# Optimization experiments

Hardware: AMD Instinct MI355X
Metric: run time of the kernel (lower is better)

The kernel has to match this reference:

```python
import jax, jax.numpy as jnp
import numpy as np
import itertools


def _rotation_perms():
    """The 24 rotation matrices of the cube, as permutations of the group
    acting on itself by left multiplication (regular action)."""
    mats = []
    for perm in itertools.permutations(range(3)):
        for signs in itertoolsools if False else itertools.product((1, -1), repeat=3):
            M = np.zeros((3, 3), dtype=np.int64)
            for r, (p, s) in enumerate(zip(perm, signs)):
                M[r, p] = s
            if int(round(np.linalg.det(M))) == 1:
                mats.append(M)
    assert len(mats) == 24
    idx = {m.tobytes(): k for k, m in enumerate(mats)}
    perms = np.zeros((24, 24), dtype=np.int64)
    for k, g in enumerate(mats):
        for i, h in enumerate(mats):
            perms[k, i] = idx[(g @ h).tobytes()]
    return perms


def compute_pair_orbits():
    all_rot = _rotation_perms()
    pair_orbit = np.full((24, 24), -1, dtype=np.int64)
    orbit_id = 0
    for i in range(24):
        for j in range(24):
            if pair_orbit[i, j] == -1:
                for g in all_rot:
                    gi, gj = int(g[i]), int(g[j])
                    if pair_orbit[gi, gj] == -1:
                        pair_orbit[gi, gj] = orbit_id
                orbit_id += 1
    assert (pair_orbit >= 0).all()
    return pair_orbit, orbit_id


C_IN, C_OUT, BATCH = 512, 512, 2048


def setup_inputs() -> dict:
    key = jax.random.key(0)
    kx, kw = jax.random.split(key)
    pair_orbit, n_orbits = compute_pair_orbits()  # (24,24), n_orbits == 24
    x = jax.random.normal(kx, (BATCH, 24, C_IN), dtype=jnp.float32)
    # kaiming-uniform-like init, bound = sqrt(6 / ((1+5) * fan_in)), fan_in = c_in*n_orbits
    bound = float(np.sqrt(1.0 / (C_IN * n_orbits)))
    weight = jax.random.uniform(kw, (C_OUT, C_IN, n_orbits), dtype=jnp.float32,
                                minval=-bound, maxval=bound)
    bias = jnp.zeros((C_OUT,), dtype=jnp.float32)
    return {"x": x, "weight": weight, "bias": bias,
            "pair_orbit": jnp.asarray(pair_orbit)}


def reference(x, weight, bias, pair_orbit):
    # kernel[o, c, i, j] = weight[o, c, pair_orbit[i, j]]
    kernel = weight[:, :, pair_orbit]            # (c_out, c_in, 24, 24)
    out = jnp.einsum('bjc,ocij->bio', x, kernel)  # (batch, 24, c_out)
    return out + bias
```

## Files before the change

kernel.cpp:

```cpp
#include <hip/hip_runtime.h>

#define BATCH 2048
#define CIN   512
#define COUT  512
#define GSZ   24
#define NORB  24
#define M_DIM (BATCH*GSZ)
#define K_DIM (GSZ*CIN)
#define N_DIM COUT
#define BM 192
#define BN 128
#define BK 64

typedef __bf16 bf16x8 __attribute__((ext_vector_type(8)));
typedef float  f32x4  __attribute__((ext_vector_type(4)));
typedef unsigned short u16;

__device__ __forceinline__ u16 f2bf(float f) {
  union { float f; unsigned u; } v; v.f = f;
  unsigned u = v.u;
  return (u16)((u + 0x7fffu + ((u >> 16) & 1u)) >> 16);
}

__global__ void convert_x(const float* __restrict__ x, u16* __restrict__ xb, int n4) {
  int t = blockIdx.x * blockDim.x + threadIdx.x;
  if (t >= n4) return;
  const float4 v = *(const float4*)(x + (size_t)t * 4);
  ushort4 o;
  o.x = f2bf(v.x); o.y = f2bf(v.y); o.z = f2bf(v.z); o.w = f2bf(v.w);
  *(ushort4*)(xb + (size_t)t * 4) = o;
}

#define TROW 520
__global__ void build_bt(const float* __restrict__ w, u16* __restrict__ bt) {
  __shared__ __align__(16) u16 lds[NORB * TROW];
  const int o = blockIdx.x;
  const int t = threadIdx.x;
  const float* wo = w + (size_t)o * K_DIM;
#pragma unroll
  for (int it = 0; it < 12; ++it) {
    const int idx = it * 256 + t;
    const float4 v = *(const float4*)(wo + idx * 4);
    const int k0 = idx * 4;
#pragma unroll
    for (int e = 0; e < 4; ++e) {
      const int k = k0 + e;
      const int c = k / 24;
      const int r = k - c * 24;
      lds[r * TROW + c] = f2bf(e == 0 ? v.x : e == 1 ? v.y : e == 2 ? v.z : v.w);
    }
  }
  __syncthreads();
  u16* bo = bt + (size_t)o * K_DIM;
#pragma unroll
  for (int it = 0; it < 6; ++it) {
    const int eidx = it * 256 + t;
    const int base = eidx * 8;
    const int r = base >> 9;
    const int c0 = base & 511;
    const uint4 v = *(const uint4*)(lds + r * TROW + c0);
    *(uint4*)(bo + base) = v;
  }
}

__launch_bounds__(256, 2)
__global__ void gemm_gc(const u16* __restrict__ xb, const u16* __restrict__ bt,
                        const float* __restrict__ bias, const int* __restrict__ pair_orbit,
                        float* __restrict__ out) {
  __shared__ __align__(16) u16 As[BM * BK];
  __shared__ __align__(16) u16 Bs[2 * BN * BK];
  __shared__ int jmap[GSZ * 25];

  const int t   = threadIdx.x;
  const int gid = blockIdx.x;
  const int xcd = gid & 7;
  const int n0  = (xcd & 3) * BN;
  const int m0  = ((gid >> 3) * 2 + (xcd >> 2)) * BM;

  for (int idx = t; idx < GSZ * NORB; idx += 256) {
    const int i = idx / 24;
    const int j = idx - i * 24;
    jmap[i * 25 + pair_orbit[idx]] = j;
  }

  const int tr0 = t >> 3;
  const int kcg = ((t & 7) ^ (tr0 & 7)) * 8;
  const u16* aSrc = xb + (size_t)(m0 + tr0) * CIN + kcg;
  const u16* bSrc = bt + (size_t)(n0 + tr0) * K_DIM + kcg;
  u16* aDst = (u16*)As + t * 8;
  u16* bDst = (u16*)Bs + t * 8;

  auto stage_a = [&](int kb) {
#pragma unroll
    for (int it = 0; it < 6; ++it)
      __builtin_amdgcn_global_load_lds(
          (__attribute__((address_space(1))) void*)(aSrc + (size_t)it * 32 * CIN + kb * 64),
          (__attribute__((address_space(3))) void*)(aDst + it * 2048), 16, 0, 0);
  };
  auto stage_b = [&](int kb, int r, int soffElems) {
#pragma unroll
    for (int it = 0; it < 4; ++it)
      __builtin_amdgcn_global_load_lds(
          (__attribute__((address_space(1))) void*)(bSrc + (size_t)it * 32 * K_DIM + r * 512 + kb * 64),
          (__attribute__((address_space(3))) void*)(bDst + soffElems + it * 2048), 16, 0, 0);
  };

  const int w    = t >> 6;
  const int lane = t & 63;
  const int lm   = lane & 15;
  const int q    = lane >> 4;
  const int mw   = (w >> 1) * 96;
  const int nw   = (w & 1) * 64;
  const int q8   = q << 3;

  int b24[6], i25[6];
#pragma unroll
  for (int f = 0; f < 6; ++f) {
    const int tr = mw + f * 16 + lm;
    const int b  = tr / 24;
    b24[f] = b * 24;
    i25[f] = (tr - b * 24) * 25;
  }
  int baseB[4];
#pragma unroll
  for (int nf = 0; nf < 4; ++nf)
    baseB[nf] = (nw + lm + 16 * nf) * 64 + (q8 ^ ((lm & 7) << 3));

  f32x4 acc[6][4];
#pragma unroll
  for (int i = 0; i < 6; ++i)
#pragma unroll
    for (int j = 0; j < 4; ++j)
      acc[i][j] = (f32x4){0.f, 0.f, 0.f, 0.f};

  stage_a(0);
  stage_b(0, 0, 0);
  __syncthreads();
  stage_b(0, 1, 8192);

  int rowC[6];
#pragma unroll
  for (int f = 0; f < 6; ++f) rowC[f] = b24[f] + jmap[i25[f]];

  for (int kb = 0; kb < 8; ++kb) {
    for (int r = 0; r < 24; ++r) {
      const int soff = (r & 1) * 8192;

      int c0[6];
#pragma unroll
      for (int f = 0; f < 6; ++f)
        c0[f] = rowC[f] * 64 + (q8 ^ ((rowC[f] & 7) << 3));

      int rowN[6];
      const int rn = (r == 23) ? 0 : (r + 1);
#pragma unroll
      for (int f = 0; f < 6; ++f) rowN[f] = b24[f] + jmap[i25[f] + rn];

#pragma unroll
      for (int h = 0; h < 2; ++h) {
        const int hx = h * 32;
        bf16x8 av[6], bv[4];
#pragma unroll
        for (int nf = 0; nf < 4; ++nf)
          bv[nf] = *(const bf16x8*)(Bs + soff + (baseB[nf] ^ hx));
#pragma unroll
        for (int f = 0; f < 6; ++f)
          av[f] = *(const bf16x8*)(As + (c0[f] ^ hx));
        __builtin_amdgcn_s_setprio(1);
#pragma unroll
        for (int mf = 0; mf < 6; ++mf)
#pragma unroll
          for (int nf = 0; nf < 4; ++nf)
            acc[mf][nf] = __builtin_amdgcn_mfma_f32_16x16x32_bf16(av[mf], bv[nf], acc[mf][nf], 0, 0, 0);
        __builtin_amdgcn_s_setprio(0);
      }

#pragma unroll
      for (int f = 0; f < 6; ++f) rowC[f] = rowN[f];

      __syncthreads();

      if (r < 22) {
        stage_b(kb, r + 2, soff);
      } else if (kb < 7) {
        if (r == 22) {
          stage_b(kb + 1, 0, soff);
        } else {
          stage_a(kb + 1);
          stage_b(kb + 1, 1, soff);
          __syncthreads();
        }
      }
    }
  }

#pragma unroll
  for (int nf = 0; nf < 4; ++nf) {
    const int col = n0 + nw + nf * 16 + lm;
    const float bv = bias[col];
#pragma unroll
    for (int mf = 0; mf < 6; ++mf) {
      const int mrow = m0 + mw + mf * 16 + q * 4;
#pragma unroll
      for (int e = 0; e < 4; ++e)
        out[(size_t)(mrow + e) * N_DIM + col] = acc[mf][nf][e] + bv;
    }
  }
}

extern "C" void kernel_launch(void* const* d_in, const int* in_sizes, int n_in,
                              void* d_out, int out_size, void* d_ws, size_t ws_size,
                              hipStream_t stream) {
  (void)in_sizes; (void)n_in; (void)out_size; (void)ws_size;
  const float* x    = (const float*)d_in[0];
  const float* wgt  = (const float*)d_in[1];
  const float* bias = (const float*)d_in[2];
  const int*   po   = (const int*)d_in[3];
  float* out = (float*)d_out;

  u16* xb = (u16*)d_ws;
  u16* bt = xb + (size_t)M_DIM * CIN;

  const int nx4 = (BATCH * GSZ * CIN) / 4;
  convert_x<<<nx4 / 256, 256, 0, stream>>>(x, xb, nx4);
  build_bt<<<COUT, 256, 0, stream>>>(wgt, bt);

  const int grid = (M_DIM / BM) * (N_DIM / BN);
  gemm_gc<<<grid, 256, 0, stream>>>(xb, bt, bias, po, out);
}
```

Measured before the change: 640.8 us.

## Switch GEMM to 32x32x16 MFMA tiles and coarsen x conversion kernel

The GEMM inner loop moves from 16x16x32 bf16 MFMA (6x4 fragments per wave) to 32x32x16 bf16 MFMA (3x2 fragments), with new LDS swizzled addressing, per-lane row gathers and epilogue mapping. Fewer, larger MFMAs cut LDS fragment reads per FLOP and instruction issue overhead. The f32-to-bf16 conversion kernel also handles four float4 per thread with a quarter of the blocks. The risk is LDS bank conflicts under the new swizzle, different register pressure, and a more scattered output store pattern.

```diff
diff --git a/kernel.cpp b/kernel.cpp
--- a/kernel.cpp
+++ b/kernel.cpp
@@ -14,6 +14,7 @@
 
 typedef __bf16 bf16x8 __attribute__((ext_vector_type(8)));
 typedef float  f32x4  __attribute__((ext_vector_type(4)));
+typedef float  f32x16 __attribute__((ext_vector_type(16)));
 typedef unsigned short u16;
 
 __device__ __forceinline__ u16 f2bf(float f) {
@@ -23,12 +24,16 @@
 }
 
 __global__ void convert_x(const float* __restrict__ x, u16* __restrict__ xb, int n4) {
-  int t = blockIdx.x * blockDim.x + threadIdx.x;
-  if (t >= n4) return;
-  const float4 v = *(const float4*)(x + (size_t)t * 4);
-  ushort4 o;
-  o.x = f2bf(v.x); o.y = f2bf(v.y); o.z = f2bf(v.z); o.w = f2bf(v.w);
-  *(ushort4*)(xb + (size_t)t * 4) = o;
+  const int base = blockIdx.x * 1024 + threadIdx.x;
+#pragma unroll
+  for (int i = 0; i < 4; ++i) {
+    const int t = base + i * 256;
+    if (t >= n4) return;
+    const float4 v = *(const float4*)(x + (size_t)t * 4);
+    ushort4 o;
+    o.x = f2bf(v.x); o.y = f2bf(v.y); o.z = f2bf(v.z); o.w = f2bf(v.w);
+    *(ushort4*)(xb + (size_t)t * 4) = o;
+  }
 }
 
 #define TROW 520
@@ -105,78 +110,89 @@
           (__attribute__((address_space(3))) void*)(bDst + soffElems + it * 2048), 16, 0, 0);
   };
 
-  const int w    = t >> 6;
-  const int lane = t & 63;
-  const int lm   = lane & 15;
-  const int q    = lane >> 4;
-  const int mw   = (w >> 1) * 96;
-  const int nw   = (w & 1) * 64;
-  const int q8   = q << 3;
-
-  int b24[6], i25[6];
-#pragma unroll
-  for (int f = 0; f < 6; ++f) {
-    const int tr = mw + f * 16 + lm;
+  const int w     = t >> 6;
+  const int lane  = t & 63;
+  const int l31   = lane & 31;
+  const int laneK = (lane >> 5) << 3;
+  const int mw    = (w >> 1) * 96;
+  const int nw    = (w & 1) * 64;
+
+  int b24[3], i25[3];
+#pragma unroll
+  for (int f = 0; f < 3; ++f) {
+    const int tr = mw + f * 32 + l31;
     const int b  = tr / 24;
     b24[f] = b * 24;
     i25[f] = (tr - b * 24) * 25;
   }
-  int baseB[4];
-#pragma unroll
-  for (int nf = 0; nf < 4; ++nf)
-    baseB[nf] = (nw + lm + 16 * nf) * 64 + (q8 ^ ((lm & 7) << 3));
-
-  f32x4 acc[6][4];
-#pragma unroll
-  for (int i = 0; i < 6; ++i)
-#pragma unroll
-    for (int j = 0; j < 4; ++j)
-      acc[i][j] = (f32x4){0.f, 0.f, 0.f, 0.f};
+  int pB[2];
+#pragma unroll
+  for (int nf = 0; nf < 2; ++nf) {
+    const int nrow = nw + nf * 32 + l31;
+    pB[nf] = (nrow << 6) ^ ((lane & 7) << 3) ^ laneK;
+  }
+
+  f32x16 acc[3][2];
+#pragma unroll
+  for (int i = 0; i < 3; ++i)
+#pragma unroll
+    for (int j = 0; j < 2; ++j)
+      acc[i][j] = (f32x16)(0.f);
 
   stage_a(0);
   stage_b(0, 0, 0);
   __syncthreads();
   stage_b(0, 1, 8192);
 
-  int rowC[6];
-#pragma unroll
-  for (int f = 0; f < 6; ++f) rowC[f] = b24[f] + jmap[i25[f]];
+  int rowC[3];
+#pragma unroll
+  for (int f = 0; f < 3; ++f) rowC[f] = b24[f] + jmap[i25[f]];
 
   for (int kb = 0; kb < 8; ++kb) {
     for (int r = 0; r < 24; ++r) {
       const int soff = (r & 1) * 8192;
 
-      int c0[6];
-#pragma unroll
-      for (int f = 0; f < 6; ++f)
-        c0[f] = rowC[f] * 64 + (q8 ^ ((rowC[f] & 7) << 3));
-
-      int rowN[6];
+      int pA[3];
+#pragma unroll
+      for (int f = 0; f < 3; ++f)
+        pA[f] = (rowC[f] << 6) ^ ((rowC[f] & 7) << 3) ^ laneK;
+
+      int rowN[3];
       const int rn = (r == 23) ? 0 : (r + 1);
 #pragma unroll
-      for (int f = 0; f < 6; ++f) rowN[f] = b24[f] + jmap[i25[f] + rn];
+      for (int f = 0; f < 3; ++f) rowN[f] = b24[f] + jmap[i25[f] + rn];
 
 #pragma unroll
       for (int h = 0; h < 2; ++h) {
-        const int hx = h * 32;
-        bf16x8 av[6], bv[4];
-#pragma unroll
-        for (int nf = 0; nf < 4; ++nf)
-          bv[nf] = *(const bf16x8*)(Bs + soff + (baseB[nf] ^ hx));
-#pragma unroll
-        for (int f = 0; f < 6; ++f)
-          av[f] = *(const bf16x8*)(As + (c0[f] ^ hx));
+        const int x0 = (2 * h) << 4;
+        const int x1 = (2 * h + 1) << 4;
+        bf16x8 av0[3], av1[3], bv0[2], bv1[2];
+#pragma unroll
+        for (int nf = 0; nf < 2; ++nf) {
+          bv0[nf] = *(const bf16x8*)(Bs + soff + (pB[nf] ^ x0));
+          bv1[nf] = *(const bf16x8*)(Bs + soff + (pB[nf] ^ x1));
+        }
+#pragma unroll
+        for (int f = 0; f < 3; ++f) {
+          av0[f] = *(const bf16x8*)(As + (pA[f] ^ x0));
+          av1[f] = *(const bf16x8*)(As + (pA[f] ^ x1));
+        }
         __builtin_amdgcn_s_setprio(1);
 #pragma unroll
-        for (int mf = 0; mf < 6; ++mf)
-#pragma unroll
-          for (int nf = 0; nf < 4; ++nf)
-            acc[mf][nf] = __builtin_amdgcn_mfma_f32_16x16x32_bf16(av[mf], bv[nf], acc[mf][nf], 0, 0, 0);
+        for (int mf = 0; mf < 3; ++mf)
+#pragma unroll
+          for (int nf = 0; nf < 2; ++nf)
+            acc[mf][nf] = __builtin_amdgcn_mfma_f32_32x32x16_bf16(av0[mf], bv0[nf], acc[mf][nf], 0, 0, 0);
+#pragma unroll
+        for (int mf = 0; mf < 3; ++mf)
+#pragma unroll
+          for (int nf = 0; nf < 2; ++nf)
+            acc[mf][nf] = __builtin_amdgcn_mfma_f32_32x32x16_bf16(av1[mf], bv1[nf], acc[mf][nf], 0, 0, 0);
         __builtin_amdgcn_s_setprio(0);
       }
 
 #pragma unroll
-      for (int f = 0; f < 6; ++f) rowC[f] = rowN[f];
+      for (int f = 0; f < 3; ++f) rowC[f] = rowN[f];
 
       __syncthreads();
 
@@ -195,15 +211,17 @@
   }
 
 #pragma unroll
-  for (int nf = 0; nf < 4; ++nf) {
-    const int col = n0 + nw + nf * 16 + lm;
+  for (int nf = 0; nf < 2; ++nf) {
+    const int col = n0 + nw + nf * 32 + l31;
     const float bv = bias[col];
 #pragma unroll
-    for (int mf = 0; mf < 6; ++mf) {
-      const int mrow = m0 + mw + mf * 16 + q * 4;
-#pragma unroll
-      for (int e = 0; e < 4; ++e)
-        out[(size_t)(mrow + e) * N_DIM + col] = acc[mf][nf][e] + bv;
+    for (int mf = 0; mf < 3; ++mf) {
+      const int rbase = m0 + mw + mf * 32 + ((lane >> 5) << 2);
+#pragma unroll
+      for (int reg = 0; reg < 16; ++reg) {
+        const int row = rbase + (reg & 3) + 8 * (reg >> 2);
+        out[(size_t)row * N_DIM + col] = acc[mf][nf][reg] + bv;
+      }
     }
   }
 }
@@ -222,7 +240,7 @@
   u16* bt = xb + (size_t)M_DIM * CIN;
 
   const int nx4 = (BATCH * GSZ * CIN) / 4;
-  convert_x<<<nx4 / 256, 256, 0, stream>>>(x, xb, nx4);
+  convert_x<<<nx4 / 1024, 256, 0, stream>>>(x, xb, nx4);
   build_bt<<<COUT, 256, 0, stream>>>(wgt, bt);
 
   const int grid = (M_DIM / BM) * (N_DIM / BN);
```

Result: slower. 713.0 us (+11.3%).

## Triple-buffer B tiles with vmcnt-based waits and one barrier per step

Applied to the files above, without the earlier changes.

The GEMM's B staging buffer grows from two to three slots, and the nested kb/r loop becomes a single flattened 192-step loop. Each step waits on the load counter with a partial `s_waitcnt vmcnt(4)`, so the newest prefetch can stay in flight while a single barrier guards the buffer. The next-but-one B tile is issued at the top of the iteration, before the MFMAs run, which lets loads overlap compute and drops one barrier per step. convert_x also processes four float4s per thread with a quarter of the blocks. The larger LDS footprint (about 75 KB per block) may limit occupancy, and the hand-written counter waits depend on exact load counts.

```diff
diff --git a/kernel.cpp b/kernel.cpp
--- a/kernel.cpp
+++ b/kernel.cpp
@@ -23,12 +23,16 @@
 }
 
 __global__ void convert_x(const float* __restrict__ x, u16* __restrict__ xb, int n4) {
-  int t = blockIdx.x * blockDim.x + threadIdx.x;
-  if (t >= n4) return;
-  const float4 v = *(const float4*)(x + (size_t)t * 4);
-  ushort4 o;
-  o.x = f2bf(v.x); o.y = f2bf(v.y); o.z = f2bf(v.z); o.w = f2bf(v.w);
-  *(ushort4*)(xb + (size_t)t * 4) = o;
+  const int base = blockIdx.x * 1024 + threadIdx.x;
+#pragma unroll
+  for (int i = 0; i < 4; ++i) {
+    const int t = base + i * 256;
+    if (t >= n4) return;
+    const float4 v = *(const float4*)(x + (size_t)t * 4);
+    ushort4 o;
+    o.x = f2bf(v.x); o.y = f2bf(v.y); o.z = f2bf(v.z); o.w = f2bf(v.w);
+    *(ushort4*)(xb + (size_t)t * 4) = o;
+  }
 }
 
 #define TROW 520
@@ -68,7 +72,7 @@
                         const float* __restrict__ bias, const int* __restrict__ pair_orbit,
                         float* __restrict__ out) {
   __shared__ __align__(16) u16 As[BM * BK];
-  __shared__ __align__(16) u16 Bs[2 * BN * BK];
+  __shared__ __align__(16) u16 Bs[3 * BN * BK];
   __shared__ int jmap[GSZ * 25];
 
   const int t   = threadIdx.x;
@@ -142,56 +146,64 @@
 #pragma unroll
   for (int f = 0; f < 6; ++f) rowC[f] = b24[f] + jmap[i25[f]];
 
-  for (int kb = 0; kb < 8; ++kb) {
-    for (int r = 0; r < 24; ++r) {
-      const int soff = (r & 1) * 8192;
-
-      int c0[6];
+  int cur = 0, w2 = 2;
+  int r2 = 2, kb2 = 0;
+  int rr = 0, kb = 0;
+
+#pragma unroll 1
+  for (int tt = 0; tt < 192; ++tt) {
+    if (tt < 191) asm volatile("s_waitcnt vmcnt(4)" ::: "memory");
+    else          asm volatile("s_waitcnt vmcnt(0)" ::: "memory");
+    __builtin_amdgcn_s_barrier();
+    __builtin_amdgcn_sched_barrier(0);
+
+    const bool bnd = (rr == 23);
+    if (!bnd && tt < 190) stage_b(kb2, r2, w2 << 13);
+
+    int c0[6];
+#pragma unroll
+    for (int f = 0; f < 6; ++f)
+      c0[f] = rowC[f] * 64 + (q8 ^ ((rowC[f] & 7) << 3));
+
+    int rowN[6];
+    const int rn = bnd ? 0 : (rr + 1);
+#pragma unroll
+    for (int f = 0; f < 6; ++f) rowN[f] = b24[f] + jmap[i25[f] + rn];
+
+    const int soff = cur << 13;
+#pragma unroll
+    for (int h = 0; h < 2; ++h) {
+      const int hx = h * 32;
+      bf16x8 av[6], bv[4];
+#pragma unroll
+      for (int nf = 0; nf < 4; ++nf)
+        bv[nf] = *(const bf16x8*)(Bs + soff + (baseB[nf] ^ hx));
 #pragma unroll
       for (int f = 0; f < 6; ++f)
-        c0[f] = rowC[f] * 64 + (q8 ^ ((rowC[f] & 7) << 3));
-
-      int rowN[6];
-      const int rn = (r == 23) ? 0 : (r + 1);
-#pragma unroll
-      for (int f = 0; f < 6; ++f) rowN[f] = b24[f] + jmap[i25[f] + rn];
-
-#pragma unroll
-      for (int h = 0; h < 2; ++h) {
-        const int hx = h * 32;
-        bf16x8 av[6], bv[4];
+        av[f] = *(const bf16x8*)(As + (c0[f] ^ hx));
+      __builtin_amdgcn_s_setprio(1);
+#pragma unroll
+      for (int mf = 0; mf < 6; ++mf)
 #pragma unroll
         for (int nf = 0; nf < 4; ++nf)
-          bv[nf] = *(const bf16x8*)(Bs + soff + (baseB[nf] ^ hx));
-#pragma unroll
-        for (int f = 0; f < 6; ++f)
-          av[f] = *(const bf16x8*)(As + (c0[f] ^ hx));
-        __builtin_amdgcn_s_setprio(1);
-#pragma unroll
-        for (int mf = 0; mf < 6; ++mf)
-#pragma unroll
-          for (int nf = 0; nf < 4; ++nf)
-            acc[mf][nf] = __builtin_amdgcn_mfma_f32_16x16x32_bf16(av[mf], bv[nf], acc[mf][nf], 0, 0, 0);
-        __builtin_amdgcn_s_setprio(0);
-      }
-
-#pragma unroll
-      for (int f = 0; f < 6; ++f) rowC[f] = rowN[f];
-
-      __syncthreads();
-
-      if (r < 22) {
-        stage_b(kb, r + 2, soff);
-      } else if (kb < 7) {
-        if (r == 22) {
-          stage_b(kb + 1, 0, soff);
-        } else {
-          stage_a(kb + 1);
-          stage_b(kb + 1, 1, soff);
-          __syncthreads();
-        }
-      }
-    }
+          acc[mf][nf] = __builtin_amdgcn_mfma_f32_16x16x32_bf16(av[mf], bv[nf], acc[mf][nf], 0, 0, 0);
+      __builtin_amdgcn_s_setprio(0);
+    }
+
+#pragma unroll
+    for (int f = 0; f < 6; ++f) rowC[f] = rowN[f];
+
+    if (bnd && kb < 7) {
+      __builtin_amdgcn_s_barrier();
+      __builtin_amdgcn_sched_barrier(0);
+      stage_a(kb + 1);
+      stage_b(kb2, r2, w2 << 13);
+    }
+
+    cur = (cur == 2) ? 0 : cur + 1;
+    w2  = (w2 == 2) ? 0 : w2 + 1;
+    if (++r2 == 24) { r2 = 0; ++kb2; }
+    if (++rr == 24) { rr = 0; ++kb; }
   }
 
 #pragma unroll
@@ -222,7 +234,7 @@
   u16* bt = xb + (size_t)M_DIM * CIN;
 
   const int nx4 = (BATCH * GSZ * CIN) / 4;
-  convert_x<<<nx4 / 256, 256, 0, stream>>>(x, xb, nx4);
+  convert_x<<<nx4 / 1024, 256, 0, stream>>>(x, xb, nx4);
   build_bt<<<COUT, 256, 0, stream>>>(wgt, bt);
 
   const int grid = (M_DIM / BM) * (N_DIM / BN);
```

Result: no change. 650.0 us (+1.4%).
